# Kernel tuning notes

Measured on AMD Instinct MI355X. Metric: run time of the kernel, lower is better.

## Reference

```python
import jax, jax.numpy as jnp
import numpy as np

N = 100000
E = 500000
LATENT = 256
EDGE_DIM = 128
HIDDEN = 2 * EDGE_DIM  # 256


def setup_inputs() -> dict:
    key = jax.random.key(0)
    k_z, k_e, k_w1, k_b1, k_w2, k_b2 = jax.random.split(key, 6)
    z = jax.random.normal(k_z, (N, LATENT), dtype=jnp.float32)
    edge_index = jax.random.randint(k_e, (2, E), 0, N, dtype=jnp.int64)
    # torch nn.Linear init: U(-1/sqrt(fan_in), 1/sqrt(fan_in))
    lim1 = 1.0 / np.sqrt(2 * LATENT)
    W1 = jax.random.uniform(k_w1, (HIDDEN, 2 * LATENT), jnp.float32, -lim1, lim1)
    b1 = jax.random.uniform(k_b1, (HIDDEN,), jnp.float32, -lim1, lim1)
    lim2 = 1.0 / np.sqrt(HIDDEN)
    W2 = jax.random.uniform(k_w2, (EDGE_DIM, HIDDEN), jnp.float32, -lim2, lim2)
    b2 = jax.random.uniform(k_b2, (EDGE_DIM,), jnp.float32, -lim2, lim2)
    return {"z": z, "edge_index": edge_index, "W1": W1, "b1": b1, "W2": W2, "b2": b2}


def reference(z, edge_index, W1, b1, W2, b2):
    # Gather endpoint embeddings and concat: [E, 2*latent]
    src = z[edge_index[0]]
    dst = z[edge_index[1]]
    pair = jnp.concatenate([src, dst], axis=1)
    # 2-layer MLP (dropout is identity in eval mode)
    h = jax.nn.relu(pair @ W1.T + b1)
    out = h @ W2.T + b2  # [E, edge_dim]
    return out
```

## Files before the change

### kernel.cpp

```cpp
#include <hip/hip_runtime.h>
#include <hip/hip_bf16.h>

#define N_NODES 100000
#define N_EDGES 500000

typedef __attribute__((ext_vector_type(8))) short  short8;
typedef __attribute__((ext_vector_type(4))) short  short4v;
typedef __attribute__((ext_vector_type(4))) float  float4v;

__device__ __forceinline__ unsigned short f2bf(float f) {
    union { float f; unsigned int u; } v; v.f = f;
    unsigned int u = v.u;
    unsigned int r = u + 0x7fffu + ((u >> 16) & 1u);
    return (unsigned short)(r >> 16);
}
__device__ __forceinline__ float bf2f(unsigned short b) {
    union { unsigned int u; float f; } v; v.u = ((unsigned int)b) << 16;
    return v.f;
}

__device__ __forceinline__ void gload_lds16(const unsigned short* g, unsigned short* l) {
    __builtin_amdgcn_global_load_lds(
        (const __attribute__((address_space(1))) unsigned int*)g,
        (__attribute__((address_space(3))) unsigned int*)l, 16, 0, 0);
}

__global__ void zconv_kernel(const float* __restrict__ z, unsigned short* __restrict__ zb) {
    size_t i = ((size_t)blockIdx.x * 256 + threadIdx.x) * 8;
    float4v a = *(const float4v*)(z + i);
    float4v b = *(const float4v*)(z + i + 4);
    short8 o;
    o[0] = (short)f2bf(a.x); o[1] = (short)f2bf(a.y); o[2] = (short)f2bf(a.z); o[3] = (short)f2bf(a.w);
    o[4] = (short)f2bf(b.x); o[5] = (short)f2bf(b.y); o[6] = (short)f2bf(b.z); o[7] = (short)f2bf(b.w);
    *(short8*)(zb + i) = o;
}

__global__ void prep_kernel(const float* __restrict__ W1, const float* __restrict__ W2,
                            unsigned short* __restrict__ w1c, unsigned short* __restrict__ w2b) {
    int j = blockIdx.x, k = threadIdx.x;
    if (j < 512) {
        float v = (j < 256) ? W1[(size_t)j * 512 + k] : W1[(size_t)(j - 256) * 512 + 256 + k];
        w1c[(size_t)j * 256 + k] = f2bf(v);
    } else {
        int o = j - 512;
        w2b[(size_t)o * 256 + k] = f2bf(W2[(size_t)o * 256 + k]);
    }
}

__launch_bounds__(256, 2)
__global__ void stage1_kernel(const unsigned short* __restrict__ zb,
                              const unsigned short* __restrict__ w1c,
                              unsigned short* __restrict__ ZW) {
    __shared__ __align__(16) unsigned short lds[32768];
    const int t    = threadIdx.x;
    const int lane = t & 63, wave = t >> 6;
    const int wm = wave >> 1, wn = wave & 1;
    const int l15 = lane & 15, quad = lane >> 4;
    const int mbase = blockIdx.x * 128, nbase = blockIdx.y * 128;

    const int lr = lane >> 3;
    const int cg = (lane & 7) ^ lr;
    const unsigned short* ag[4]; const unsigned short* bg[4];
    int lo[4];
#pragma unroll
    for (int q = 0; q < 4; ++q) {
        int rA = wave * 32 + q * 8 + lr;
        int gA = mbase + rA; if (gA >= N_NODES) gA = N_NODES - 1;
        ag[q] = zb  + (size_t)gA * 256 + cg * 8;
        bg[q] = w1c + (size_t)(nbase + rA) * 256 + cg * 8;
        lo[q] = (wave * 4 + q) * 512 + lane * 8;
    }

    float4v acc[4][4];
    const float4v fz = {0.f, 0.f, 0.f, 0.f};
#pragma unroll
    for (int i = 0; i < 4; ++i)
#pragma unroll
        for (int j = 0; j < 4; ++j) acc[i][j] = fz;

#pragma unroll
    for (int q = 0; q < 4; ++q) gload_lds16(ag[q], lds + lo[q]);
#pragma unroll
    for (int q = 0; q < 4; ++q) gload_lds16(bg[q], lds + 8192 + lo[q]);
    __builtin_amdgcn_sched_barrier(0);
    asm volatile("s_waitcnt vmcnt(0)" ::: "memory");
    __builtin_amdgcn_s_barrier();
    __builtin_amdgcn_sched_barrier(0);

    for (int ks = 0; ks < 4; ++ks) {
        const int cur = ks & 1;
        const unsigned short* At = lds + cur * 16384;
        const unsigned short* Bt = At + 8192;
        if (ks < 3) {
            unsigned short* nb = lds + (cur ^ 1) * 16384;
            const int kk = (ks + 1) * 64;
#pragma unroll
            for (int q = 0; q < 4; ++q) gload_lds16(ag[q] + kk, nb + lo[q]);
#pragma unroll
            for (int q = 0; q < 4; ++q) gload_lds16(bg[q] + kk, nb + 8192 + lo[q]);
        }
        __builtin_amdgcn_sched_barrier(0);

#pragma unroll
        for (int s = 0; s < 2; ++s) {
            const int ch = ((s * 4 + quad) ^ (l15 & 7)) * 8;
            short8 af[4], bfr[4];
#pragma unroll
            for (int i = 0; i < 4; ++i)
                af[i] = *(const short8*)(At + (wm * 64 + i * 16 + l15) * 64 + ch);
#pragma unroll
            for (int j = 0; j < 4; ++j)
                bfr[j] = *(const short8*)(Bt + (wn * 64 + j * 16 + l15) * 64 + ch);
#pragma unroll
            for (int i = 0; i < 4; ++i)
#pragma unroll
                for (int j = 0; j < 4; ++j)
                    acc[i][j] = __builtin_amdgcn_mfma_f32_16x16x32_bf16(af[i], bfr[j], acc[i][j], 0, 0, 0);
        }
        __builtin_amdgcn_sched_barrier(0);
        asm volatile("s_waitcnt vmcnt(0)" ::: "memory");
        __builtin_amdgcn_s_barrier();
        __builtin_amdgcn_sched_barrier(0);
    }

#pragma unroll
    for (int i = 0; i < 4; ++i)
#pragma unroll
        for (int j = 0; j < 4; ++j) {
            int row = wm * 64 + i * 16 + quad * 4;
            int col = wn * 64 + j * 16 + l15;
#pragma unroll
            for (int r = 0; r < 4; ++r)
                lds[(row + r) * 136 + col] = f2bf(acc[i][j][r]);
        }
    __syncthreads();
    for (int c = t; c < 128 * 16; c += 256) {
        int row = c >> 4, ch2 = c & 15;
        int grow = mbase + row;
        if (grow < N_NODES)
            *(short8*)(ZW + (size_t)grow * 512 + nbase + ch2 * 8) =
                *(const short8*)(lds + row * 136 + ch2 * 8);
    }
}

#define H_PITCH 264
#define EBLK 32
#define NT 8
__launch_bounds__(256, 3)
__global__ void stage2_kernel(const int* __restrict__ eidx, const unsigned short* __restrict__ ZW,
                              const float* __restrict__ b1, const unsigned short* __restrict__ w2b,
                              const float* __restrict__ b2, float* __restrict__ out) {
    __shared__ unsigned short h[EBLK * H_PITCH];
    __shared__ int idx2[512];
    float* hf = (float*)h;

    const int t    = threadIdx.x;
    const int lane = t & 63, wave = t >> 6;
    const int lj = lane & 31, hi = lane >> 5;
    const int l15 = lane & 15, quad = lane >> 4;
    const int w8 = wave * 8;
    const int eb0 = blockIdx.x * (EBLK * NT);

    {
        int e = eb0 + t; if (e >= N_EDGES) e = N_EDGES - 1;
        idx2[t]       = eidx[e];
        idx2[256 + t] = eidx[N_EDGES + e];
    }
    __syncthreads();

    short8 bfrag[2][8];
#pragma unroll
    for (int jj = 0; jj < 2; ++jj)
#pragma unroll
        for (int kk = 0; kk < 8; ++kk)
            bfrag[jj][kk] = *(const short8*)(w2b + (size_t)(wave * 32 + jj * 16 + l15) * 256
                                             + kk * 32 + quad * 8);

    float4v b1a = *(const float4v*)(b1 + lj * 8);
    float4v b1b = *(const float4v*)(b1 + lj * 8 + 4);
    float b2r[2];
#pragma unroll
    for (int jj = 0; jj < 2; ++jj) b2r[jj] = b2[wave * 32 + jj * 16 + l15];
    const unsigned short* zs = ZW + lj * 8;
    const unsigned short* zd = ZW + 256 + lj * 8;

    short8 va[4], vb[4];
#pragma unroll
    for (int p = 0; p < 4; ++p) {
        int r = w8 + p * 2 + hi;
        va[p] = *(const short8*)(zs + (size_t)idx2[r] * 512);
        vb[p] = *(const short8*)(zd + (size_t)idx2[256 + r] * 512);
    }
    __builtin_amdgcn_sched_barrier(0);

    for (int tt = 0; tt < NT; ++tt) {
        const int tb = tt * 32;
#pragma unroll
        for (int p = 0; p < 4; ++p) {
            int r = w8 + p * 2 + hi;
            short8 xa = va[p], xb = vb[p];
            short8 rv;
#pragma unroll
            for (int i = 0; i < 8; ++i) {
                float v = bf2f((unsigned short)xa[i]) + bf2f((unsigned short)xb[i])
                        + ((i < 4) ? b1a[i] : b1b[i - 4]);
                v = v > 0.f ? v : 0.f;
                rv[i] = (short)f2bf(v);
            }
            *(short8*)(h + r * H_PITCH + lj * 8) = rv;
        }
        if (tt + 1 < NT) {
            const int tb2 = tb + 32;
#pragma unroll
            for (int p = 0; p < 4; ++p) {
                int r = tb2 + w8 + p * 2 + hi;
                va[p] = *(const short8*)(zs + (size_t)idx2[r] * 512);
                vb[p] = *(const short8*)(zd + (size_t)idx2[256 + r] * 512);
            }
        }
        __builtin_amdgcn_sched_barrier(0);
        asm volatile("s_waitcnt lgkmcnt(0)" ::: "memory");
        __builtin_amdgcn_s_barrier();
        __builtin_amdgcn_sched_barrier(0);
        float4v acc[2][2];
        const float4v fz = {0.f, 0.f, 0.f, 0.f};
        acc[0][0] = fz; acc[0][1] = fz; acc[1][0] = fz; acc[1][1] = fz;
#pragma unroll
        for (int kk = 0; kk < 8; ++kk) {
            short8 af0 = *(const short8*)(h + (l15)      * H_PITCH + kk * 32 + quad * 8);
            short8 af1 = *(const short8*)(h + (16 + l15) * H_PITCH + kk * 32 + quad * 8);
            acc[0][0] = __builtin_amdgcn_mfma_f32_16x16x32_bf16(af0, bfrag[0][kk], acc[0][0], 0, 0, 0);
            acc[0][1] = __builtin_amdgcn_mfma_f32_16x16x32_bf16(af0, bfrag[1][kk], acc[0][1], 0, 0, 0);
            acc[1][0] = __builtin_amdgcn_mfma_f32_16x16x32_bf16(af1, bfrag[0][kk], acc[1][0], 0, 0, 0);
            acc[1][1] = __builtin_amdgcn_mfma_f32_16x16x32_bf16(af1, bfrag[1][kk], acc[1][1], 0, 0, 0);
        }
        __builtin_amdgcn_sched_barrier(0);
        __builtin_amdgcn_s_barrier();
        __builtin_amdgcn_sched_barrier(0);
#pragma unroll
        for (int jj = 0; jj < 2; ++jj)
#pragma unroll
            for (int i = 0; i < 2; ++i)
#pragma unroll
                for (int r = 0; r < 4; ++r)
                    hf[(i * 16 + quad * 4 + r) * 132 + wave * 32 + jj * 16 + l15] =
                        acc[i][jj][r] + b2r[jj];
        asm volatile("s_waitcnt lgkmcnt(0)" ::: "memory");
        __builtin_amdgcn_s_barrier();
        __builtin_amdgcn_sched_barrier(0);
#pragma unroll
        for (int pass = 0; pass < 4; ++pass) {
            int it = pass * 256 + t;
            int row = it >> 5, c4 = (it & 31) * 4;
            int e = eb0 + tb + row;
            if (e < N_EDGES) {
                float4v v = *(const float4v*)(hf + row * 132 + c4);
                __builtin_nontemporal_store(v, (float4v*)(out + (size_t)e * 128 + c4));
            }
        }
        __builtin_amdgcn_sched_barrier(0);
        __builtin_amdgcn_s_barrier();
        __builtin_amdgcn_sched_barrier(0);
    }
}

__global__ void fallback_kernel(const float* __restrict__ z, const int* __restrict__ eidx,
                                const float* __restrict__ W1, const float* __restrict__ b1,
                                const float* __restrict__ W2, const float* __restrict__ b2,
                                float* __restrict__ out) {
    __shared__ float zs[512];
    __shared__ float hh[256];
    int e = blockIdx.x, t = threadIdx.x;
    int s = eidx[e], d = eidx[N_EDGES + e];
    zs[t]       = z[(size_t)s * 256 + t];
    zs[256 + t] = z[(size_t)d * 256 + t];
    __syncthreads();
    float a = b1[t];
    const float* wr = W1 + (size_t)t * 512;
    for (int k = 0; k < 512; ++k) a += zs[k] * wr[k];
    hh[t] = a > 0.f ? a : 0.f;
    __syncthreads();
    if (t < 128) {
        float o = b2[t];
        const float* w2r = W2 + (size_t)t * 256;
        for (int k = 0; k < 256; ++k) o += hh[k] * w2r[k];
        out[(size_t)e * 128 + t] = o;
    }
}

extern "C" void kernel_launch(void* const* d_in, const int* in_sizes, int n_in,
                              void* d_out, int out_size, void* d_ws, size_t ws_size,
                              hipStream_t stream) {
    const float* z    = (const float*)d_in[0];
    const int*   eidx = (const int*)d_in[1];
    const float* W1   = (const float*)d_in[2];
    const float* b1   = (const float*)d_in[3];
    const float* W2   = (const float*)d_in[4];
    const float* b2   = (const float*)d_in[5];
    float* out = (float*)d_out;

    const size_t zw_bytes = (size_t)N_NODES * 512 * 2;
    const size_t w1c_off  = zw_bytes;
    const size_t w2b_off  = w1c_off + (size_t)512 * 256 * 2;
    const size_t need     = w2b_off + (size_t)128 * 256 * 2;

    if (ws_size < need) {
        fallback_kernel<<<N_EDGES, 256, 0, stream>>>(z, eidx, W1, b1, W2, b2, out);
        return;
    }
    unsigned short* ZW  = (unsigned short*)d_ws;
    unsigned short* w1c = (unsigned short*)((char*)d_ws + w1c_off);
    unsigned short* w2b = (unsigned short*)((char*)d_ws + w2b_off);
    unsigned short* zb  = (unsigned short*)d_out;

    zconv_kernel<<<12500, 256, 0, stream>>>(z, zb);
    prep_kernel<<<640, 256, 0, stream>>>(W1, W2, w1c, w2b);
    stage1_kernel<<<dim3(782, 4), 256, 0, stream>>>(zb, w1c, ZW);
    const int s2_blocks = (N_EDGES + EBLK * NT - 1) / (EBLK * NT);
    stage2_kernel<<<s2_blocks, 256, 0, stream>>>(eidx, ZW, b1, w2b, b2, out);
}
```

Baseline: 453.9 us.

## Make stage1 GEMM persistent with cross-tile prefetch and direct register stores

Stage1 now launches 122x4 persistent blocks, each looping over a contiguous range of M tiles. The first K-slice of the next tile is prefetched during the last K step of the current one, which removes per-block prologue stalls. Swapping the MFMA operand order transposes the accumulator layout, so results are written straight from registers as 4-element bf16 vectors instead of being staged through LDS with a barrier. The trade-off is fewer blocks (488), which may leave some CUs idle or unbalanced, and smaller, less coalesced global stores.

```diff
diff --git a/kernel.cpp b/kernel.cpp
--- a/kernel.cpp
+++ b/kernel.cpp
@@ -47,6 +47,8 @@
     }
 }
 
+#define S1_NXB 122
+#define S1_MT_TOTAL 782
 __launch_bounds__(256, 2)
 __global__ void stage1_kernel(const unsigned short* __restrict__ zb,
                               const unsigned short* __restrict__ w1c,
@@ -56,90 +58,98 @@
     const int lane = t & 63, wave = t >> 6;
     const int wm = wave >> 1, wn = wave & 1;
     const int l15 = lane & 15, quad = lane >> 4;
-    const int mbase = blockIdx.x * 128, nbase = blockIdx.y * 128;
+    const int nbase = blockIdx.y * 128;
+
+    const int bx = blockIdx.x;
+    const int t0 = (bx * S1_MT_TOTAL) / S1_NXB;
+    const int t1 = ((bx + 1) * S1_MT_TOTAL) / S1_NXB;
+    const int MTb = t1 - t0;
 
     const int lr = lane >> 3;
     const int cg = (lane & 7) ^ lr;
-    const unsigned short* ag[4]; const unsigned short* bg[4];
-    int lo[4];
+    int rowoff[4]; int lo[4]; const unsigned short* bgq[4];
 #pragma unroll
     for (int q = 0; q < 4; ++q) {
-        int rA = wave * 32 + q * 8 + lr;
-        int gA = mbase + rA; if (gA >= N_NODES) gA = N_NODES - 1;
-        ag[q] = zb  + (size_t)gA * 256 + cg * 8;
-        bg[q] = w1c + (size_t)(nbase + rA) * 256 + cg * 8;
-        lo[q] = (wave * 4 + q) * 512 + lane * 8;
-    }
-
-    float4v acc[4][4];
-    const float4v fz = {0.f, 0.f, 0.f, 0.f};
-#pragma unroll
-    for (int i = 0; i < 4; ++i)
-#pragma unroll
-        for (int j = 0; j < 4; ++j) acc[i][j] = fz;
-
-#pragma unroll
-    for (int q = 0; q < 4; ++q) gload_lds16(ag[q], lds + lo[q]);
-#pragma unroll
-    for (int q = 0; q < 4; ++q) gload_lds16(bg[q], lds + 8192 + lo[q]);
+        rowoff[q] = wave * 32 + q * 8 + lr;
+        lo[q]     = (wave * 4 + q) * 512 + lane * 8;
+        bgq[q]    = w1c + (size_t)(nbase + rowoff[q]) * 256 + cg * 8;
+    }
+
+    auto stage = [&](int buf, int mt, int kk) {
+        unsigned short* A = lds + buf * 16384;
+        unsigned short* B = A + 8192;
+        const int mbase = mt * 128;
+#pragma unroll
+        for (int q = 0; q < 4; ++q) {
+            int gA = mbase + rowoff[q]; if (gA >= N_NODES) gA = N_NODES - 1;
+            gload_lds16(zb + (size_t)gA * 256 + cg * 8 + kk, A + lo[q]);
+        }
+#pragma unroll
+        for (int q = 0; q < 4; ++q)
+            gload_lds16(bgq[q] + kk, B + lo[q]);
+    };
+
+    stage(0, t0, 0);
     __builtin_amdgcn_sched_barrier(0);
     asm volatile("s_waitcnt vmcnt(0)" ::: "memory");
     __builtin_amdgcn_s_barrier();
     __builtin_amdgcn_sched_barrier(0);
 
-    for (int ks = 0; ks < 4; ++ks) {
-        const int cur = ks & 1;
-        const unsigned short* At = lds + cur * 16384;
-        const unsigned short* Bt = At + 8192;
-        if (ks < 3) {
-            unsigned short* nb = lds + (cur ^ 1) * 16384;
-            const int kk = (ks + 1) * 64;
-#pragma unroll
-            for (int q = 0; q < 4; ++q) gload_lds16(ag[q] + kk, nb + lo[q]);
-#pragma unroll
-            for (int q = 0; q < 4; ++q) gload_lds16(bg[q] + kk, nb + 8192 + lo[q]);
-        }
-        __builtin_amdgcn_sched_barrier(0);
-
-#pragma unroll
-        for (int s = 0; s < 2; ++s) {
-            const int ch = ((s * 4 + quad) ^ (l15 & 7)) * 8;
-            short8 af[4], bfr[4];
-#pragma unroll
-            for (int i = 0; i < 4; ++i)
-                af[i] = *(const short8*)(At + (wm * 64 + i * 16 + l15) * 64 + ch);
-#pragma unroll
-            for (int j = 0; j < 4; ++j)
-                bfr[j] = *(const short8*)(Bt + (wn * 64 + j * 16 + l15) * 64 + ch);
-#pragma unroll
-            for (int i = 0; i < 4; ++i)
+    float4v acc[4][4];
+    const float4v fz = {0.f, 0.f, 0.f, 0.f};
+
+    for (int mt = 0; mt < MTb; ++mt) {
+#pragma unroll
+        for (int i = 0; i < 4; ++i)
+#pragma unroll
+            for (int j = 0; j < 4; ++j) acc[i][j] = fz;
+
+#pragma unroll
+        for (int k4 = 0; k4 < 4; ++k4) {
+            if (!(k4 == 3 && mt == MTb - 1))
+                stage((k4 & 1) ^ 1, t0 + mt + (k4 == 3 ? 1 : 0), ((k4 + 1) & 3) * 64);
+            __builtin_amdgcn_sched_barrier(0);
+
+            const unsigned short* At = lds + (k4 & 1) * 16384;
+            const unsigned short* Bt = At + 8192;
+#pragma unroll
+            for (int s2 = 0; s2 < 2; ++s2) {
+                const int ch = ((s2 * 4 + quad) ^ (l15 & 7)) * 8;
+                short8 af[4], bfr[4];
+#pragma unroll
+                for (int i = 0; i < 4; ++i)
+                    af[i] = *(const short8*)(At + (wm * 64 + i * 16 + l15) * 64 + ch);
 #pragma unroll
                 for (int j = 0; j < 4; ++j)
-                    acc[i][j] = __builtin_amdgcn_mfma_f32_16x16x32_bf16(af[i], bfr[j], acc[i][j], 0, 0, 0);
-        }
-        __builtin_amdgcn_sched_barrier(0);
-        asm volatile("s_waitcnt vmcnt(0)" ::: "memory");
-        __builtin_amdgcn_s_barrier();
-        __builtin_amdgcn_sched_barrier(0);
-    }
-
-#pragma unroll
-    for (int i = 0; i < 4; ++i)
-#pragma unroll
-        for (int j = 0; j < 4; ++j) {
-            int row = wm * 64 + i * 16 + quad * 4;
-            int col = wn * 64 + j * 16 + l15;
-#pragma unroll
-            for (int r = 0; r < 4; ++r)
-                lds[(row + r) * 136 + col] = f2bf(acc[i][j][r]);
-        }
-    __syncthreads();
-    for (int c = t; c < 128 * 16; c += 256) {
-        int row = c >> 4, ch2 = c & 15;
-        int grow = mbase + row;
-        if (grow < N_NODES)
-            *(short8*)(ZW + (size_t)grow * 512 + nbase + ch2 * 8) =
-                *(const short8*)(lds + row * 136 + ch2 * 8);
+                    bfr[j] = *(const short8*)(Bt + (wn * 64 + j * 16 + l15) * 64 + ch);
+#pragma unroll
+                for (int i = 0; i < 4; ++i)
+#pragma unroll
+                    for (int j = 0; j < 4; ++j)
+                        acc[i][j] = __builtin_amdgcn_mfma_f32_16x16x32_bf16(bfr[j], af[i], acc[i][j], 0, 0, 0);
+            }
+            __builtin_amdgcn_sched_barrier(0);
+            asm volatile("s_waitcnt vmcnt(0)" ::: "memory");
+            __builtin_amdgcn_s_barrier();
+            __builtin_amdgcn_sched_barrier(0);
+        }
+
+        const int mbase = (t0 + mt) * 128;
+#pragma unroll
+        for (int i = 0; i < 4; ++i) {
+            int grow = mbase + wm * 64 + i * 16 + l15;
+            if (grow < N_NODES) {
+#pragma unroll
+                for (int j = 0; j < 4; ++j) {
+                    short4v o;
+                    o[0] = (short)f2bf(acc[i][j][0]);
+                    o[1] = (short)f2bf(acc[i][j][1]);
+                    o[2] = (short)f2bf(acc[i][j][2]);
+                    o[3] = (short)f2bf(acc[i][j][3]);
+                    *(short4v*)(ZW + (size_t)grow * 512 + nbase + wn * 64 + j * 16 + quad * 4) = o;
+                }
+            }
+        }
     }
 }
 
@@ -315,7 +325,7 @@
 
     zconv_kernel<<<12500, 256, 0, stream>>>(z, zb);
     prep_kernel<<<640, 256, 0, stream>>>(W1, W2, w1c, w2b);
-    stage1_kernel<<<dim3(782, 4), 256, 0, stream>>>(zb, w1c, ZW);
+    stage1_kernel<<<dim3(S1_NXB, 4), 256, 0, stream>>>(zb, w1c, ZW);
     const int s2_blocks = (N_EDGES + EBLK * NT - 1) / (EBLK * NT);
     stage2_kernel<<<s2_blocks, 256, 0, stream>>>(eidx, ZW, b1, w2b, b2, out);
 }
```

Result: no change. 460.1 us (+1.4%).
